# Kernel optimization log

Measured on AMD Instinct MI355X. Metric: run time of the kernel, lower is better.

Reference implementation:

```python
import jax, jax.numpy as jnp
import numpy as np

B, S, H = 2, 2048, 2048
NH, G = 32, 8
D = H // NH          # head dim = 64
R = NH // G          # q heads per kv group = 4
SCALE = 1.0 / np.sqrt(D)


def setup_inputs() -> dict:
    key = jax.random.key(0)
    ks = jax.random.split(key, 9)
    s = 0.02
    return {
        "x": jax.random.normal(ks[0], (B, S, H), jnp.float32),
        "Wq": jax.random.normal(ks[1], (H, H), jnp.float32) * s,
        "bq": jnp.zeros((H,), jnp.float32),
        "Wk": jax.random.normal(ks[2], (H, G * D), jnp.float32) * s,
        "bk": jnp.zeros((G * D,), jnp.float32),
        "Wv": jax.random.normal(ks[3], (H, G * D), jnp.float32) * s,
        "bv": jnp.zeros((G * D,), jnp.float32),
        "Wo": jax.random.normal(ks[4], (H, H), jnp.float32) * s,
        "bo": jnp.zeros((H,), jnp.float32),
    }


def reference(x, Wq, bq, Wk, bk, Wv, bv, Wo, bo):
    # projections
    q = x @ Wq + bq                                  # [B,S,H]
    k = x @ Wk + bk                                  # [B,S,G*D]
    v = x @ Wv + bv                                  # [B,S,G*D]
    # split heads: q -> [B,G,R,S,D]; k,v -> [B,G,S,D]
    q = q.reshape(B, S, G, R, D).transpose(0, 2, 3, 1, 4)
    k = k.reshape(B, S, G, D).transpose(0, 2, 1, 3)
    v = v.reshape(B, S, G, D).transpose(0, 2, 1, 3)
    # grouped attention without materializing expanded KV
    scores = jnp.einsum('bgrqd,bgkd->bgrqk', q, k) * SCALE   # [B,G,R,S,S]
    weights = jax.nn.softmax(scores, axis=-1)
    out = jnp.einsum('bgrqk,bgkd->bgrqd', weights, v)        # [B,G,R,S,D]
    # merge heads: head index = g*R + r (matches torch expand/reshape order)
    out = out.transpose(0, 3, 1, 2, 4).reshape(B, S, H)
    return out @ Wo + bo
```

## Files before the change

### kernel.cpp

```cpp
#include <hip/hip_runtime.h>
#include <stdint.h>

#define S_LEN 2048
#define HDIM  2048
#define BATCH 2
#define NKV   8
#define GD    512
#define MROWS 4096
#define NQKV  3072

typedef __attribute__((ext_vector_type(8))) __bf16 bf16x8;
typedef __attribute__((ext_vector_type(4))) float f32x4;
typedef __attribute__((ext_vector_type(16))) float f32x16;
typedef unsigned short u16;

__device__ __forceinline__ u16 bfc(float f) {
  union { __bf16 b; u16 u; } v; v.b = (__bf16)f; return v.u;
}
__device__ __forceinline__ int cvtpk(float lo, float hi) {
  int r; asm("v_cvt_pk_bf16_f32 %0, %1, %2" : "=v"(r) : "v"(lo), "v"(hi)); return r;
}

__device__ __forceinline__ void glds16(const void* g, void* lds) {
  __builtin_amdgcn_global_load_lds((const __attribute__((address_space(1))) void*)g,
                                   (__attribute__((address_space(3))) void*)lds, 16, 0, 0);
}

__global__ __launch_bounds__(256) void cvt_f32_bf16_kernel(const float* __restrict__ x,
                                                           u16* __restrict__ y, int n4) {
  int i = blockIdx.x * 256 + threadIdx.x;
  if (i >= n4) return;
  const float4 v = ((const float4*)x)[i];
  ushort4 o;
  o.x = bfc(v.x); o.y = bfc(v.y); o.z = bfc(v.z); o.w = bfc(v.w);
  ((ushort4*)y)[i] = o;
}

__global__ __launch_bounds__(256) void concat_bias_kernel(const float* __restrict__ bq,
                                                          const float* __restrict__ bk,
                                                          const float* __restrict__ bv,
                                                          float* __restrict__ o) {
  int i = blockIdx.x * 256 + threadIdx.x;
  if (i < HDIM) o[i] = bq[i];
  else if (i < HDIM + GD) o[i] = bk[i - HDIM];
  else if (i < NQKV) o[i] = bv[i - HDIM - GD];
}

__global__ __launch_bounds__(256) void transpose_f32_bf16(const float* __restrict__ W,
                                                          u16* __restrict__ Wt,
                                                          int Rr, int Cc) {
  __shared__ float t[32][33];
  int bx = blockIdx.x * 32;
  int by = blockIdx.y * 32;
  int tx = threadIdx.x & 31, ty = threadIdx.x >> 5;
#pragma unroll
  for (int i = 0; i < 4; ++i)
    t[ty + i * 8][tx] = W[(size_t)(by + ty + i * 8) * Cc + bx + tx];
  __syncthreads();
#pragma unroll
  for (int i = 0; i < 4; ++i)
    Wt[(size_t)(bx + ty + i * 8) * Rr + by + tx] = bfc(t[tx][ty + i * 8]);
}

__global__ __launch_bounds__(256) void transpose_v_kernel(const u16* __restrict__ QKV,
                                                          u16* __restrict__ Vt) {
  __shared__ u16 t[32][33];
  int b = blockIdx.z;
  const u16* Vb = QKV + (size_t)b * S_LEN * NQKV + HDIM + GD;
  u16* Vtb = Vt + (size_t)b * GD * S_LEN;
  int bx = blockIdx.x * 32;
  int by = blockIdx.y * 32;
  int tx = threadIdx.x & 31, ty = threadIdx.x >> 5;
#pragma unroll
  for (int i = 0; i < 4; ++i)
    t[ty + i * 8][tx] = Vb[(size_t)(by + ty + i * 8) * NQKV + bx + tx];
  __syncthreads();
#pragma unroll
  for (int i = 0; i < 4; ++i)
    Vtb[(size_t)(bx + ty + i * 8) * S_LEN + by + tx] = t[tx][ty + i * 8];
}

__global__ __launch_bounds__(256) void gemm_bf16(const u16* __restrict__ A,
                                                 const u16* __restrict__ Bt,
                                                 const float* __restrict__ bias,
                                                 void* __restrict__ C,
                                                 int M, int N, int K,
                                                 float alphaA, float alphaB, int qlim,
                                                 int obf) {
  __shared__ __attribute__((aligned(16))) u16 As[128 * 32];
  __shared__ __attribute__((aligned(16))) u16 Bs[128 * 32];
  const int tid = threadIdx.x, lane = tid & 63, wv = tid >> 6;
  const int wr = wv >> 1, wc = wv & 1;
  const int r16 = lane & 15, kg = lane >> 4;

  const int nwg = gridDim.x * gridDim.y;
  const int orig = blockIdx.y * gridDim.x + blockIdx.x;
  const int qq = nwg >> 3, rr = nwg & 7;
  const int xcd = orig & 7, loc = orig >> 3;
  const int swz = (xcd < rr ? xcd * (qq + 1) : rr * (qq + 1) + (xcd - rr) * qq) + loc;
  const int m0 = (swz / gridDim.x) * 128, n0 = (swz % gridDim.x) * 128;
  const float alpha = (n0 < qlim) ? alphaA : alphaB;

  f32x4 acc[4][4];
#pragma unroll
  for (int m = 0; m < 4; ++m)
#pragma unroll
    for (int n = 0; n < 4; ++n) acc[m][n] = (f32x4)0.0f;

  auto stage = [&](int k0) {
#pragma unroll
    for (int i = 0; i < 2; ++i) {
      int chunk = i * 256 + wv * 64 + lane;
      int row = chunk >> 2, cc = chunk & 3;
      glds16(A + (size_t)(m0 + row) * K + k0 + cc * 8, &As[(i * 256 + wv * 64) * 8]);
    }
#pragma unroll
    for (int i = 0; i < 2; ++i) {
      int chunk = i * 256 + wv * 64 + lane;
      int row = chunk >> 2, cc = chunk & 3;
      glds16(Bt + (size_t)(n0 + row) * K + k0 + cc * 8, &Bs[(i * 256 + wv * 64) * 8]);
    }
  };

  stage(0);
  const int nk = K / 32;
  for (int kt = 0; kt < nk; ++kt) {
    asm volatile("s_waitcnt vmcnt(0)" ::: "memory");
    __syncthreads();
    bf16x8 af[4], bfr[4];
#pragma unroll
    for (int m = 0; m < 4; ++m)
      af[m] = *(const bf16x8*)&As[(wr * 64 + m * 16 + r16) * 32 + kg * 8];
#pragma unroll
    for (int n = 0; n < 4; ++n)
      bfr[n] = *(const bf16x8*)&Bs[(wc * 64 + n * 16 + r16) * 32 + kg * 8];
    __syncthreads();
    if (kt + 1 < nk) stage((kt + 1) * 32);
#pragma unroll
    for (int m = 0; m < 4; ++m)
#pragma unroll
      for (int n = 0; n < 4; ++n)
        acc[m][n] = __builtin_amdgcn_mfma_f32_16x16x32_bf16(af[m], bfr[n], acc[m][n], 0, 0, 0);
  }

#pragma unroll
  for (int m = 0; m < 4; ++m) {
    int row = m0 + wr * 64 + m * 16 + kg * 4;
#pragma unroll
    for (int n = 0; n < 4; ++n) {
      int col = n0 + wc * 64 + n * 16 + r16;
      float bb = bias ? bias[col] : 0.0f;
#pragma unroll
      for (int i = 0; i < 4; ++i) {
        float val = (acc[m][n][i] + bb) * alpha;
        if (obf) ((u16*)C)[(size_t)(row + i) * N + col] = bfc(val);
        else     ((float*)C)[(size_t)(row + i) * N + col] = val;
      }
    }
  }
}

__global__ __launch_bounds__(256, 4) void gqa_attn_kernel(const u16* __restrict__ qkv,
                                                          const u16* __restrict__ vT,
                                                          u16* __restrict__ att) {
  __shared__ __attribute__((aligned(16))) u16 Ks[2][64 * 64];
  __shared__ __attribute__((aligned(16))) u16 Vs[2][64 * 64];

  const int bid = blockIdx.x;
  const int qt = bid & 15;
  const int h = (bid >> 4) & 31;
  const int b = bid >> 9;
  const int g = h >> 2;
  const int tid = threadIdx.x, lane = tid & 63, wv = tid >> 6;
  const int q31 = lane & 31, hi = lane >> 5;
  const int qbase = qt * 128 + wv * 32;

  const u16* qrow = qkv + (size_t)(b * S_LEN + qbase + q31) * NQKV + h * 64;
  bf16x8 qf[4];
#pragma unroll
  for (int d = 0; d < 4; ++d)
    qf[d] = *(const bf16x8*)(qrow + d * 16 + hi * 8);

  union { u16 w[8]; bf16x8 v; } uo;
#pragma unroll
  for (int i = 0; i < 8; ++i) uo.w[i] = 0x3F80;
  const bf16x8 onesf = uo.v;

  const u16* kbase = qkv + (size_t)(b * S_LEN) * NQKV + HDIM + g * 64;
  const u16* vbase = vT + (size_t)((b * NKV + g) * 64) * S_LEN;

  auto stageK = [&](int t, int buf) {
    const int kk0 = t * 64;
#pragma unroll
    for (int i = 0; i < 2; ++i) {
      int chunk = i * 256 + wv * 64 + lane;
      int row = chunk >> 3, cc = chunk & 7;
      int cs = cc ^ (row & 7);
      glds16(kbase + (size_t)(kk0 + row) * NQKV + cs * 8, &Ks[buf][(i * 256 + wv * 64) * 8]);
      glds16(vbase + (size_t)row * S_LEN + kk0 + cs * 8, &Vs[buf][(i * 256 + wv * 64) * 8]);
    }
  };

  f32x16 o0 = (f32x16)0.0f, o1 = (f32x16)0.0f, ol = (f32x16)0.0f;

  stageK(0, 0);
  const int sw = q31 & 7;
  const int NT = S_LEN / 64;
  for (int t = 0; t < NT; ++t) {
    const int cur = t & 1;
    if (t + 1 < NT) {
      stageK(t + 1, cur ^ 1);
      asm volatile("s_waitcnt vmcnt(4)" ::: "memory");
    } else {
      asm volatile("s_waitcnt vmcnt(0)" ::: "memory");
    }
    __builtin_amdgcn_s_barrier();
    asm volatile("" ::: "memory");

    f32x16 p0 = (f32x16)0.0f, p1 = (f32x16)0.0f;
    __builtin_amdgcn_s_setprio(1);
#pragma unroll
    for (int d = 0; d < 4; ++d) {
      int ch = ((d * 2 + hi) ^ sw) * 8;
      bf16x8 kf0 = *(const bf16x8*)&Ks[cur][q31 * 64 + ch];
      bf16x8 kf1 = *(const bf16x8*)&Ks[cur][(32 + q31) * 64 + ch];
      p0 = __builtin_amdgcn_mfma_f32_32x32x16_bf16(kf0, qf[d], p0, 0, 0, 0);
      p1 = __builtin_amdgcn_mfma_f32_32x32x16_bf16(kf1, qf[d], p1, 0, 0, 0);
    }
    __builtin_amdgcn_s_setprio(0);

#pragma unroll
    for (int r = 0; r < 16; ++r) {
      p0[r] = exp2f(p0[r]);
      p1[r] = exp2f(p1[r]);
    }

    bf16x8 pa[4];
#pragma unroll
    for (int kk = 0; kk < 2; ++kk) {
      int w0 = cvtpk(p0[kk * 8 + 0], p0[kk * 8 + 1]);
      int w1 = cvtpk(p0[kk * 8 + 2], p0[kk * 8 + 3]);
      int w2 = cvtpk(p0[kk * 8 + 4], p0[kk * 8 + 5]);
      int w3 = cvtpk(p0[kk * 8 + 6], p0[kk * 8 + 7]);
      auto s0 = __builtin_amdgcn_permlane32_swap(w0, w2, false, false);
      auto s1 = __builtin_amdgcn_permlane32_swap(w1, w3, false, false);
      union { int w[4]; bf16x8 v; } u;
      u.w[0] = s0[0]; u.w[1] = s1[0]; u.w[2] = s0[1]; u.w[3] = s1[1];
      pa[kk] = u.v;
    }
#pragma unroll
    for (int kk = 0; kk < 2; ++kk) {
      int w0 = cvtpk(p1[kk * 8 + 0], p1[kk * 8 + 1]);
      int w1 = cvtpk(p1[kk * 8 + 2], p1[kk * 8 + 3]);
      int w2 = cvtpk(p1[kk * 8 + 4], p1[kk * 8 + 5]);
      int w3 = cvtpk(p1[kk * 8 + 6], p1[kk * 8 + 7]);
      auto s0 = __builtin_amdgcn_permlane32_swap(w0, w2, false, false);
      auto s1 = __builtin_amdgcn_permlane32_swap(w1, w3, false, false);
      union { int w[4]; bf16x8 v; } u;
      u.w[0] = s0[0]; u.w[1] = s1[0]; u.w[2] = s0[1]; u.w[3] = s1[1];
      pa[2 + kk] = u.v;
    }

    __builtin_amdgcn_s_setprio(1);
#pragma unroll
    for (int ks = 0; ks < 4; ++ks) {
      int ch = (((ks * 2 + hi)) ^ sw) * 8;
      bf16x8 vf0 = *(const bf16x8*)&Vs[cur][q31 * 64 + ch];
      bf16x8 vf1 = *(const bf16x8*)&Vs[cur][(32 + q31) * 64 + ch];
      o0 = __builtin_amdgcn_mfma_f32_32x32x16_bf16(pa[ks], vf0, o0, 0, 0, 0);
      o1 = __builtin_amdgcn_mfma_f32_32x32x16_bf16(pa[ks], vf1, o1, 0, 0, 0);
      ol = __builtin_amdgcn_mfma_f32_32x32x16_bf16(pa[ks], onesf, ol, 0, 0, 0);
    }
    __builtin_amdgcn_s_setprio(0);
    asm volatile("" ::: "memory");
    __builtin_amdgcn_s_barrier();
    asm volatile("" ::: "memory");
  }

  u16* obase = att + (size_t)(b * S_LEN + qbase) * HDIM + h * 64 + q31;
#pragma unroll
  for (int r = 0; r < 16; ++r) {
    int qq2 = (r & 3) + 8 * (r >> 2) + 4 * hi;
    float inv = 1.0f / ol[r];
    obase[(size_t)qq2 * HDIM]      = bfc(o0[r] * inv);
    obase[(size_t)qq2 * HDIM + 32] = bfc(o1[r] * inv);
  }
}

extern "C" void kernel_launch(void* const* d_in, const int* in_sizes, int n_in,
                              void* d_out, int out_size, void* d_ws, size_t ws_size,
                              hipStream_t stream) {
  const float* x  = (const float*)d_in[0];
  const float* Wq = (const float*)d_in[1];
  const float* bq = (const float*)d_in[2];
  const float* Wk = (const float*)d_in[3];
  const float* bk = (const float*)d_in[4];
  const float* Wv = (const float*)d_in[5];
  const float* bv = (const float*)d_in[6];
  const float* Wo = (const float*)d_in[7];
  const float* bo = (const float*)d_in[8];
  float* out = (float*)d_out;

  char* p = (char*)d_ws;
  u16* xb    = (u16*)p; p += (size_t)MROWS * HDIM * 2;
  u16* wqkvT = (u16*)p; p += (size_t)NQKV * HDIM * 2;
  u16* woT   = (u16*)p; p += (size_t)HDIM * HDIM * 2;
  float* bqkv = (float*)p; p += (size_t)NQKV * 4;
  u16* qkv   = (u16*)p; p += (size_t)MROWS * NQKV * 2;
  u16* vtb   = (u16*)p; p += (size_t)MROWS * GD * 2;
  u16* attb  = (u16*)p; p += (size_t)MROWS * HDIM * 2;

  const float aQ = 0.18033688011112042f;

  cvt_f32_bf16_kernel<<<(MROWS * HDIM / 4 + 255) / 256, 256, 0, stream>>>(x, xb, MROWS * HDIM / 4);
  transpose_f32_bf16<<<dim3(HDIM / 32, HDIM / 32), 256, 0, stream>>>(Wq, wqkvT, HDIM, HDIM);
  transpose_f32_bf16<<<dim3(GD / 32, HDIM / 32), 256, 0, stream>>>(Wk, wqkvT + (size_t)HDIM * HDIM, HDIM, GD);
  transpose_f32_bf16<<<dim3(GD / 32, HDIM / 32), 256, 0, stream>>>(Wv, wqkvT + (size_t)(HDIM + GD) * HDIM, HDIM, GD);
  transpose_f32_bf16<<<dim3(HDIM / 32, HDIM / 32), 256, 0, stream>>>(Wo, woT, HDIM, HDIM);
  concat_bias_kernel<<<(NQKV + 255) / 256, 256, 0, stream>>>(bq, bk, bv, bqkv);
  gemm_bf16<<<dim3(NQKV / 128, MROWS / 128), 256, 0, stream>>>(xb, wqkvT, bqkv, qkv,
                                                               MROWS, NQKV, HDIM, aQ, 1.0f, HDIM, 1);
  transpose_v_kernel<<<dim3(GD / 32, S_LEN / 32, BATCH), 256, 0, stream>>>(qkv, vtb);
  gqa_attn_kernel<<<BATCH * 32 * 16, 256, 0, stream>>>(qkv, vtb, attb);
  gemm_bf16<<<dim3(HDIM / 128, MROWS / 128), 256, 0, stream>>>(attb, woT, bo, out,
                                                               MROWS, HDIM, HDIM, 1.0f, 1.0f, HDIM, 0);
}
```

Before: 243.8 us.

## Fuse x fp32-to-bf16 conversion into QKV GEMM and merge weight prep kernels

The QKV GEMM now reads x in fp32 directly through registers, converts it to bf16 with packed convert instructions and writes it to LDS. This removes the separate conversion kernel and its round trip through a bf16 copy of x. The four weight transposes and the bias concat are merged into one launch, which cuts launch overhead. In exchange, the A operand is no longer loaded asynchronously into LDS: each iteration waits on vmcnt(0), which may expose more load latency inside the GEMM. The GEMM also reads twice as many bytes for A.

Result: no change. 247.5 us (+1.5%).

```diff
diff --git a/kernel.cpp b/kernel.cpp
--- a/kernel.cpp
+++ b/kernel.cpp
@@ -26,32 +26,33 @@
                                    (__attribute__((address_space(3))) void*)lds, 16, 0, 0);
 }
 
-__global__ __launch_bounds__(256) void cvt_f32_bf16_kernel(const float* __restrict__ x,
-                                                           u16* __restrict__ y, int n4) {
-  int i = blockIdx.x * 256 + threadIdx.x;
-  if (i >= n4) return;
-  const float4 v = ((const float4*)x)[i];
-  ushort4 o;
-  o.x = bfc(v.x); o.y = bfc(v.y); o.z = bfc(v.z); o.w = bfc(v.w);
-  ((ushort4*)y)[i] = o;
-}
-
-__global__ __launch_bounds__(256) void concat_bias_kernel(const float* __restrict__ bq,
-                                                          const float* __restrict__ bk,
-                                                          const float* __restrict__ bv,
-                                                          float* __restrict__ o) {
-  int i = blockIdx.x * 256 + threadIdx.x;
-  if (i < HDIM) o[i] = bq[i];
-  else if (i < HDIM + GD) o[i] = bk[i - HDIM];
-  else if (i < NQKV) o[i] = bv[i - HDIM - GD];
-}
-
-__global__ __launch_bounds__(256) void transpose_f32_bf16(const float* __restrict__ W,
-                                                          u16* __restrict__ Wt,
-                                                          int Rr, int Cc) {
+__global__ __launch_bounds__(256) void transpose_all(const float* __restrict__ Wq,
+                                                     const float* __restrict__ Wk,
+                                                     const float* __restrict__ Wv,
+                                                     const float* __restrict__ Wo,
+                                                     const float* __restrict__ bq,
+                                                     const float* __restrict__ bk,
+                                                     const float* __restrict__ bv,
+                                                     u16* __restrict__ wqkvT,
+                                                     u16* __restrict__ woT,
+                                                     float* __restrict__ bqkv) {
+  const int bid = blockIdx.x;
+  if (bid >= 10240) {
+    int i = (bid - 10240) * 256 + threadIdx.x;
+    if (i < HDIM) bqkv[i] = bq[i];
+    else if (i < HDIM + GD) bqkv[i] = bk[i - HDIM];
+    else if (i < NQKV) bqkv[i] = bv[i - HDIM - GD];
+    return;
+  }
+  const float* W; u16* Wt; int Cc, idx;
+  if (bid < 4096)      { W = Wq; Wt = wqkvT;                              Cc = HDIM; idx = bid; }
+  else if (bid < 5120) { W = Wk; Wt = wqkvT + (size_t)HDIM * HDIM;        Cc = GD;   idx = bid - 4096; }
+  else if (bid < 6144) { W = Wv; Wt = wqkvT + (size_t)(HDIM + GD) * HDIM; Cc = GD;   idx = bid - 5120; }
+  else                 { W = Wo; Wt = woT;                                Cc = HDIM; idx = bid - 6144; }
+  const int gx = Cc / 32;
+  const int bx = (idx % gx) * 32, by = (idx / gx) * 32;
+
   __shared__ float t[32][33];
-  int bx = blockIdx.x * 32;
-  int by = blockIdx.y * 32;
   int tx = threadIdx.x & 31, ty = threadIdx.x >> 5;
 #pragma unroll
   for (int i = 0; i < 4; ++i)
@@ -59,7 +60,7 @@
   __syncthreads();
 #pragma unroll
   for (int i = 0; i < 4; ++i)
-    Wt[(size_t)(bx + ty + i * 8) * Rr + by + tx] = bfc(t[tx][ty + i * 8]);
+    Wt[(size_t)(bx + ty + i * 8) * HDIM + by + tx] = bfc(t[tx][ty + i * 8]);
 }
 
 __global__ __launch_bounds__(256) void transpose_v_kernel(const u16* __restrict__ QKV,
@@ -80,13 +81,12 @@
     Vtb[(size_t)(bx + ty + i * 8) * S_LEN + by + tx] = t[tx][ty + i * 8];
 }
 
-__global__ __launch_bounds__(256) void gemm_bf16(const u16* __restrict__ A,
-                                                 const u16* __restrict__ Bt,
-                                                 const float* __restrict__ bias,
-                                                 void* __restrict__ C,
-                                                 int M, int N, int K,
-                                                 float alphaA, float alphaB, int qlim,
-                                                 int obf) {
+__global__ __launch_bounds__(256) void gemm_qkv(const float* __restrict__ A,
+                                                const u16* __restrict__ Bt,
+                                                const float* __restrict__ bias,
+                                                u16* __restrict__ C,
+                                                int M, int N, int K,
+                                                float alphaA, float alphaB, int qlim) {
   __shared__ __attribute__((aligned(16))) u16 As[128 * 32];
   __shared__ __attribute__((aligned(16))) u16 Bs[128 * 32];
   const int tid = threadIdx.x, lane = tid & 63, wv = tid >> 6;
@@ -101,6 +101,88 @@
   const int m0 = (swz / gridDim.x) * 128, n0 = (swz % gridDim.x) * 128;
   const float alpha = (n0 < qlim) ? alphaA : alphaB;
 
+  const int arow = tid >> 1, ahr = (tid & 1) * 16;
+
+  f32x4 acc[4][4];
+#pragma unroll
+  for (int m = 0; m < 4; ++m)
+#pragma unroll
+    for (int n = 0; n < 4; ++n) acc[m][n] = (f32x4)0.0f;
+
+  float4 ar[4];
+  auto issueA = [&](int k0) {
+    const float4* ap = (const float4*)(A + (size_t)(m0 + arow) * K + k0 + ahr);
+    ar[0] = ap[0]; ar[1] = ap[1]; ar[2] = ap[2]; ar[3] = ap[3];
+  };
+  auto stageB = [&](int k0) {
+#pragma unroll
+    for (int i = 0; i < 2; ++i) {
+      int chunk = i * 256 + wv * 64 + lane;
+      int row = chunk >> 2, cc = chunk & 3;
+      glds16(Bt + (size_t)(n0 + row) * K + k0 + cc * 8, &Bs[(i * 256 + wv * 64) * 8]);
+    }
+  };
+
+  issueA(0);
+  stageB(0);
+  const int nk = K / 32;
+  for (int kt = 0; kt < nk; ++kt) {
+    asm volatile("s_waitcnt vmcnt(0)" ::: "memory");
+    union { int w[8]; bf16x8 v[2]; } pk;
+    const float* fr = (const float*)ar;
+#pragma unroll
+    for (int j = 0; j < 8; ++j) pk.w[j] = cvtpk(fr[2 * j], fr[2 * j + 1]);
+    *(bf16x8*)&As[arow * 32 + ahr] = pk.v[0];
+    *(bf16x8*)&As[arow * 32 + ahr + 8] = pk.v[1];
+    __syncthreads();
+    bf16x8 af[4], bfr[4];
+#pragma unroll
+    for (int m = 0; m < 4; ++m)
+      af[m] = *(const bf16x8*)&As[(wr * 64 + m * 16 + r16) * 32 + kg * 8];
+#pragma unroll
+    for (int n = 0; n < 4; ++n)
+      bfr[n] = *(const bf16x8*)&Bs[(wc * 64 + n * 16 + r16) * 32 + kg * 8];
+    __syncthreads();
+    if (kt + 1 < nk) { issueA((kt + 1) * 32); stageB((kt + 1) * 32); }
+#pragma unroll
+    for (int m = 0; m < 4; ++m)
+#pragma unroll
+      for (int n = 0; n < 4; ++n)
+        acc[m][n] = __builtin_amdgcn_mfma_f32_16x16x32_bf16(af[m], bfr[n], acc[m][n], 0, 0, 0);
+  }
+
+#pragma unroll
+  for (int m = 0; m < 4; ++m) {
+    int row = m0 + wr * 64 + m * 16 + kg * 4;
+#pragma unroll
+    for (int n = 0; n < 4; ++n) {
+      int col = n0 + wc * 64 + n * 16 + r16;
+      float bb = bias[col];
+#pragma unroll
+      for (int i = 0; i < 4; ++i)
+        C[(size_t)(row + i) * N + col] = bfc((acc[m][n][i] + bb) * alpha);
+    }
+  }
+}
+
+__global__ __launch_bounds__(256) void gemm_bf16(const u16* __restrict__ A,
+                                                 const u16* __restrict__ Bt,
+                                                 const float* __restrict__ bias,
+                                                 float* __restrict__ C,
+                                                 int M, int N, int K) {
+  __shared__ __attribute__((aligned(16))) u16 As[128 * 32];
+  __shared__ __attribute__((aligned(16))) u16 Bs[128 * 32];
+  const int tid = threadIdx.x, lane = tid & 63, wv = tid >> 6;
+  const int wr = wv >> 1, wc = wv & 1;
+  const int r16 = lane & 15, kg = lane >> 4;
+
+  const int nwg = gridDim.x * gridDim.y;
+  const int orig = blockIdx.y * gridDim.x + blockIdx.x;
+  const int qq = nwg >> 3, rr = nwg & 7;
+  const int xcd = orig & 7, loc = orig >> 3;
+  const int swz = (xcd < rr ? xcd * (qq + 1) : rr * (qq + 1) + (xcd - rr) * qq) + loc;
+  const int m0 = (swz / gridDim.x) * 128, n0 = (swz % gridDim.x) * 128;
+
   f32x4 acc[4][4];
 #pragma unroll
   for (int m = 0; m < 4; ++m)
@@ -149,13 +231,10 @@
 #pragma unroll
     for (int n = 0; n < 4; ++n) {
       int col = n0 + wc * 64 + n * 16 + r16;
-      float bb = bias ? bias[col] : 0.0f;
-#pragma unroll
-      for (int i = 0; i < 4; ++i) {
-        float val = (acc[m][n][i] + bb) * alpha;
-        if (obf) ((u16*)C)[(size_t)(row + i) * N + col] = bfc(val);
-        else     ((float*)C)[(size_t)(row + i) * N + col] = val;
-      }
+      float bb = bias[col];
+#pragma unroll
+      for (int i = 0; i < 4; ++i)
+        C[(size_t)(row + i) * N + col] = acc[m][n][i] + bb;
     }
   }
 }
@@ -302,7 +381,6 @@
   float* out = (float*)d_out;
 
   char* p = (char*)d_ws;
-  u16* xb    = (u16*)p; p += (size_t)MROWS * HDIM * 2;
   u16* wqkvT = (u16*)p; p += (size_t)NQKV * HDIM * 2;
   u16* woT   = (u16*)p; p += (size_t)HDIM * HDIM * 2;
   float* bqkv = (float*)p; p += (size_t)NQKV * 4;
@@ -312,16 +390,11 @@
 
   const float aQ = 0.18033688011112042f;
 
-  cvt_f32_bf16_kernel<<<(MROWS * HDIM / 4 + 255) / 256, 256, 0, stream>>>(x, xb, MROWS * HDIM / 4);
-  transpose_f32_bf16<<<dim3(HDIM / 32, HDIM / 32), 256, 0, stream>>>(Wq, wqkvT, HDIM, HDIM);
-  transpose_f32_bf16<<<dim3(GD / 32, HDIM / 32), 256, 0, stream>>>(Wk, wqkvT + (size_t)HDIM * HDIM, HDIM, GD);
-  transpose_f32_bf16<<<dim3(GD / 32, HDIM / 32), 256, 0, stream>>>(Wv, wqkvT + (size_t)(HDIM + GD) * HDIM, HDIM, GD);
-  transpose_f32_bf16<<<dim3(HDIM / 32, HDIM / 32), 256, 0, stream>>>(Wo, woT, HDIM, HDIM);
-  concat_bias_kernel<<<(NQKV + 255) / 256, 256, 0, stream>>>(bq, bk, bv, bqkv);
-  gemm_bf16<<<dim3(NQKV / 128, MROWS / 128), 256, 0, stream>>>(xb, wqkvT, bqkv, qkv,
-                                                               MROWS, NQKV, HDIM, aQ, 1.0f, HDIM, 1);
+  transpose_all<<<10252, 256, 0, stream>>>(Wq, Wk, Wv, Wo, bq, bk, bv, wqkvT, woT, bqkv);
+  gemm_qkv<<<dim3(NQKV / 128, MROWS / 128), 256, 0, stream>>>(x, wqkvT, bqkv, qkv,
+                                                              MROWS, NQKV, HDIM, aQ, 1.0f, HDIM);
   transpose_v_kernel<<<dim3(GD / 32, S_LEN / 32, BATCH), 256, 0, stream>>>(qkv, vtb);
   gqa_attn_kernel<<<BATCH * 32 * 16, 256, 0, stream>>>(qkv, vtb, attb);
   gemm_bf16<<<dim3(HDIM / 128, MROWS / 128), 256, 0, stream>>>(attb, woT, bo, out,
-                                                               MROWS, HDIM, HDIM, 1.0f, 1.0f, HDIM, 0);
-}
+                                                               MROWS, HDIM, HDIM);
+}
```

## Software-pipeline QK^T one tile ahead in attention and merge weight-prep launches

Applied to the files above, without the earlier changes.

The attention loop now computes the next tile's QK^T scores while the current tile's exp and PV products run, with separate K and V staging and K loaded two tiles ahead. This is meant to overlap MFMA work with softmax VALU work and hide load latency. The occupancy hint drops from 4 to 2 blocks per CU, since the extra score accumulators raise register use. The four weight transposes and the bias concat are merged into one launch to cut launch overhead. The prologue contains a redundant warm-up MFMA loop whose results are discarded.

Result: no change. 239.5 us (-1.7%).

```diff
diff --git a/kernel.cpp b/kernel.cpp
--- a/kernel.cpp
+++ b/kernel.cpp
@@ -36,22 +36,33 @@
   ((ushort4*)y)[i] = o;
 }
 
-__global__ __launch_bounds__(256) void concat_bias_kernel(const float* __restrict__ bq,
-                                                          const float* __restrict__ bk,
-                                                          const float* __restrict__ bv,
-                                                          float* __restrict__ o) {
-  int i = blockIdx.x * 256 + threadIdx.x;
-  if (i < HDIM) o[i] = bq[i];
-  else if (i < HDIM + GD) o[i] = bk[i - HDIM];
-  else if (i < NQKV) o[i] = bv[i - HDIM - GD];
-}
-
-__global__ __launch_bounds__(256) void transpose_f32_bf16(const float* __restrict__ W,
-                                                          u16* __restrict__ Wt,
-                                                          int Rr, int Cc) {
+__global__ __launch_bounds__(256) void transpose_all(const float* __restrict__ Wq,
+                                                     const float* __restrict__ Wk,
+                                                     const float* __restrict__ Wv,
+                                                     const float* __restrict__ Wo,
+                                                     const float* __restrict__ bq,
+                                                     const float* __restrict__ bk,
+                                                     const float* __restrict__ bv,
+                                                     u16* __restrict__ wqkvT,
+                                                     u16* __restrict__ woT,
+                                                     float* __restrict__ bqkv) {
+  const int bid = blockIdx.x;
+  if (bid >= 10240) {
+    int i = (bid - 10240) * 256 + threadIdx.x;
+    if (i < HDIM) bqkv[i] = bq[i];
+    else if (i < HDIM + GD) bqkv[i] = bk[i - HDIM];
+    else if (i < NQKV) bqkv[i] = bv[i - HDIM - GD];
+    return;
+  }
+  const float* W; u16* Wt; int Cc, idx;
+  if (bid < 4096)      { W = Wq; Wt = wqkvT;                              Cc = HDIM; idx = bid; }
+  else if (bid < 5120) { W = Wk; Wt = wqkvT + (size_t)HDIM * HDIM;        Cc = GD;   idx = bid - 4096; }
+  else if (bid < 6144) { W = Wv; Wt = wqkvT + (size_t)(HDIM + GD) * HDIM; Cc = GD;   idx = bid - 5120; }
+  else                 { W = Wo; Wt = woT;                                Cc = HDIM; idx = bid - 6144; }
+  const int gx = Cc / 32;
+  const int bx = (idx % gx) * 32, by = (idx / gx) * 32;
+
   __shared__ float t[32][33];
-  int bx = blockIdx.x * 32;
-  int by = blockIdx.y * 32;
   int tx = threadIdx.x & 31, ty = threadIdx.x >> 5;
 #pragma unroll
   for (int i = 0; i < 4; ++i)
@@ -59,7 +70,7 @@
   __syncthreads();
 #pragma unroll
   for (int i = 0; i < 4; ++i)
-    Wt[(size_t)(bx + ty + i * 8) * Rr + by + tx] = bfc(t[tx][ty + i * 8]);
+    Wt[(size_t)(bx + ty + i * 8) * HDIM + by + tx] = bfc(t[tx][ty + i * 8]);
 }
 
 __global__ __launch_bounds__(256) void transpose_v_kernel(const u16* __restrict__ QKV,
@@ -160,7 +171,7 @@
   }
 }
 
-__global__ __launch_bounds__(256, 4) void gqa_attn_kernel(const u16* __restrict__ qkv,
+__global__ __launch_bounds__(256, 2) void gqa_attn_kernel(const u16* __restrict__ qkv,
                                                           const u16* __restrict__ vT,
                                                           u16* __restrict__ att) {
   __shared__ __attribute__((aligned(16))) u16 Ks[2][64 * 64];
@@ -189,52 +200,84 @@
   const u16* kbase = qkv + (size_t)(b * S_LEN) * NQKV + HDIM + g * 64;
   const u16* vbase = vT + (size_t)((b * NKV + g) * 64) * S_LEN;
 
-  auto stageK = [&](int t, int buf) {
+  auto stageKo = [&](int t) {
     const int kk0 = t * 64;
 #pragma unroll
     for (int i = 0; i < 2; ++i) {
       int chunk = i * 256 + wv * 64 + lane;
       int row = chunk >> 3, cc = chunk & 7;
       int cs = cc ^ (row & 7);
-      glds16(kbase + (size_t)(kk0 + row) * NQKV + cs * 8, &Ks[buf][(i * 256 + wv * 64) * 8]);
-      glds16(vbase + (size_t)row * S_LEN + kk0 + cs * 8, &Vs[buf][(i * 256 + wv * 64) * 8]);
+      glds16(kbase + (size_t)(kk0 + row) * NQKV + cs * 8, &Ks[t & 1][(i * 256 + wv * 64) * 8]);
     }
   };
+  auto stageVo = [&](int t) {
+    const int kk0 = t * 64;
+#pragma unroll
+    for (int i = 0; i < 2; ++i) {
+      int chunk = i * 256 + wv * 64 + lane;
+      int row = chunk >> 3, cc = chunk & 7;
+      int cs = cc ^ (row & 7);
+      glds16(vbase + (size_t)row * S_LEN + kk0 + cs * 8, &Vs[t & 1][(i * 256 + wv * 64) * 8]);
+    }
+  };
 
   f32x16 o0 = (f32x16)0.0f, o1 = (f32x16)0.0f, ol = (f32x16)0.0f;
-
-  stageK(0, 0);
   const int sw = q31 & 7;
   const int NT = S_LEN / 64;
+
+  stageKo(0); stageVo(0); stageKo(1);
+  asm volatile("s_waitcnt vmcnt(4)" ::: "memory");
+  __builtin_amdgcn_s_barrier();
+  asm volatile("" ::: "memory");
+  f32x16 p0 = (f32x16)0.0f, p1 = (f32x16)0.0f;
+#pragma unroll
+  for (int d = 0; d < 4; ++d) {
+    int ch = ((d * 2 + hi) ^ sw) * 8;
+    bf16x8 kf0 = *(const bf16x8*)&Ks[0][q31 * 64 + ch];
+    bf16x8 kf1 = *(const bf16x8*)&Ks[0][(32 + q31) * 64 + ch];
+    p0 = __builtin_amdgcn_mfma_f32_32x32x16_bf16(kf0, qf[0 + 0], p0, 0, 0, 0);
+    p1 = __builtin_amdgcn_mfma_f32_32x32x16_bf16(kf1, qf[0 + 0], p1, 0, 0, 0);
+    (void)0;
+  }
+  p0 = (f32x16)0.0f; p1 = (f32x16)0.0f;
+#pragma unroll
+  for (int d = 0; d < 4; ++d) {
+    int ch = ((d * 2 + hi) ^ sw) * 8;
+    bf16x8 kf0 = *(const bf16x8*)&Ks[0][q31 * 64 + ch];
+    bf16x8 kf1 = *(const bf16x8*)&Ks[0][(32 + q31) * 64 + ch];
+    p0 = __builtin_amdgcn_mfma_f32_32x32x16_bf16(kf0, qf[d], p0, 0, 0, 0);
+    p1 = __builtin_amdgcn_mfma_f32_32x32x16_bf16(kf1, qf[d], p1, 0, 0, 0);
+  }
+  asm volatile("" ::: "memory");
+  __builtin_amdgcn_s_barrier();
+  asm volatile("" ::: "memory");
+
   for (int t = 0; t < NT; ++t) {
-    const int cur = t & 1;
-    if (t + 1 < NT) {
-      stageK(t + 1, cur ^ 1);
-      asm volatile("s_waitcnt vmcnt(4)" ::: "memory");
-    } else {
-      asm volatile("s_waitcnt vmcnt(0)" ::: "memory");
-    }
+    if (t + 2 < NT) stageKo(t + 2);
+    if (t + 1 < NT) stageVo(t + 1);
+    if (t + 2 < NT)      asm volatile("s_waitcnt vmcnt(4)" ::: "memory");
+    else if (t + 1 < NT) asm volatile("s_waitcnt vmcnt(2)" ::: "memory");
+    else                 asm volatile("s_waitcnt vmcnt(0)" ::: "memory");
     __builtin_amdgcn_s_barrier();
     asm volatile("" ::: "memory");
 
-    f32x16 p0 = (f32x16)0.0f, p1 = (f32x16)0.0f;
-    __builtin_amdgcn_s_setprio(1);
-#pragma unroll
-    for (int d = 0; d < 4; ++d) {
-      int ch = ((d * 2 + hi) ^ sw) * 8;
-      bf16x8 kf0 = *(const bf16x8*)&Ks[cur][q31 * 64 + ch];
-      bf16x8 kf1 = *(const bf16x8*)&Ks[cur][(32 + q31) * 64 + ch];
-      p0 = __builtin_amdgcn_mfma_f32_32x32x16_bf16(kf0, qf[d], p0, 0, 0, 0);
-      p1 = __builtin_amdgcn_mfma_f32_32x32x16_bf16(kf1, qf[d], p1, 0, 0, 0);
-    }
-    __builtin_amdgcn_s_setprio(0);
-
+    f32x16 n0 = (f32x16)0.0f, n1 = (f32x16)0.0f;
+    if (t + 1 < NT) {
+      const u16* Kc = Ks[(t + 1) & 1];
+#pragma unroll
+      for (int d = 0; d < 4; ++d) {
+        int ch = ((d * 2 + hi) ^ sw) * 8;
+        bf16x8 kf0 = *(const bf16x8*)&Kc[q31 * 64 + ch];
+        bf16x8 kf1 = *(const bf16x8*)&Kc[(32 + q31) * 64 + ch];
+        n0 = __builtin_amdgcn_mfma_f32_32x32x16_bf16(kf0, qf[d], n0, 0, 0, 0);
+        n1 = __builtin_amdgcn_mfma_f32_32x32x16_bf16(kf1, qf[d], n1, 0, 0, 0);
+      }
+    }
 #pragma unroll
     for (int r = 0; r < 16; ++r) {
       p0[r] = exp2f(p0[r]);
       p1[r] = exp2f(p1[r]);
     }
-
     bf16x8 pa[4];
 #pragma unroll
     for (int kk = 0; kk < 2; ++kk) {
@@ -261,12 +304,13 @@
       pa[2 + kk] = u.v;
     }
 
+    const u16* Vc = Vs[t & 1];
     __builtin_amdgcn_s_setprio(1);
 #pragma unroll
     for (int ks = 0; ks < 4; ++ks) {
-      int ch = (((ks * 2 + hi)) ^ sw) * 8;
-      bf16x8 vf0 = *(const bf16x8*)&Vs[cur][q31 * 64 + ch];
-      bf16x8 vf1 = *(const bf16x8*)&Vs[cur][(32 + q31) * 64 + ch];
+      int ch = ((ks * 2 + hi) ^ sw) * 8;
+      bf16x8 vf0 = *(const bf16x8*)&Vc[q31 * 64 + ch];
+      bf16x8 vf1 = *(const bf16x8*)&Vc[(32 + q31) * 64 + ch];
       o0 = __builtin_amdgcn_mfma_f32_32x32x16_bf16(pa[ks], vf0, o0, 0, 0, 0);
       o1 = __builtin_amdgcn_mfma_f32_32x32x16_bf16(pa[ks], vf1, o1, 0, 0, 0);
       ol = __builtin_amdgcn_mfma_f32_32x32x16_bf16(pa[ks], onesf, ol, 0, 0, 0);
@@ -275,6 +319,8 @@
     asm volatile("" ::: "memory");
     __builtin_amdgcn_s_barrier();
     asm volatile("" ::: "memory");
+
+    p0 = n0; p1 = n1;
   }
 
   u16* obase = att + (size_t)(b * S_LEN + qbase) * HDIM + h * 64 + q31;
@@ -313,11 +359,7 @@
   const float aQ = 0.18033688011112042f;
 
   cvt_f32_bf16_kernel<<<(MROWS * HDIM / 4 + 255) / 256, 256, 0, stream>>>(x, xb, MROWS * HDIM / 4);
-  transpose_f32_bf16<<<dim3(HDIM / 32, HDIM / 32), 256, 0, stream>>>(Wq, wqkvT, HDIM, HDIM);
-  transpose_f32_bf16<<<dim3(GD / 32, HDIM / 32), 256, 0, stream>>>(Wk, wqkvT + (size_t)HDIM * HDIM, HDIM, GD);
-  transpose_f32_bf16<<<dim3(GD / 32, HDIM / 32), 256, 0, stream>>>(Wv, wqkvT + (size_t)(HDIM + GD) * HDIM, HDIM, GD);
-  transpose_f32_bf16<<<dim3(HDIM / 32, HDIM / 32), 256, 0, stream>>>(Wo, woT, HDIM, HDIM);
-  concat_bias_kernel<<<(NQKV + 255) / 256, 256, 0, stream>>>(bq, bk, bv, bqkv);
+  transpose_all<<<10252, 256, 0, stream>>>(Wq, Wk, Wv, Wo, bq, bk, bv, wqkvT, woT, bqkv);
   gemm_bf16<<<dim3(NQKV / 128, MROWS / 128), 256, 0, stream>>>(xb, wqkvT, bqkv, qkv,
                                                                MROWS, NQKV, HDIM, aQ, 1.0f, HDIM, 1);
   transpose_v_kernel<<<dim3(GD / 32, S_LEN / 32, BATCH), 256, 0, stream>>>(qkv, vtb);
```
